# Performance work log

Hardware: AMD Instinct MI355X
Metric: run time of the kernel (lower is better)

## Reference

```python
import jax, jax.numpy as jnp
import numpy as np
from jax import lax

B, CIN, COUT, K = 4, 128, 128, 3
Z = X = Y = 32
EPS = 1e-8


def setup_inputs() -> dict:
    key = jax.random.key(0)
    k1, k2, k3 = jax.random.split(key, 3)
    x = jax.random.normal(k1, (B, CIN, Z, X, Y), dtype=jnp.float32)
    S = jax.random.normal(k2, (B, CIN), dtype=jnp.float32)
    weight = jax.random.normal(k3, (COUT, CIN, K, K, K), dtype=jnp.float32)
    return {"x": x, "S": S, "weight": weight}


def reference(x, S, weight):
    b, cin, z, xx, yy = x.shape
    cout = weight.shape[0]
    # Per-sample modulated weight: [B, cout, cin, k, k, k]
    W = weight[None] * (S[:, None, :, None, None, None] + 1.0)
    # Demodulation: L2-normalize each (b, cout) filter
    d = lax.rsqrt(jnp.sum(W * W, axis=(2, 3, 4, 5), keepdims=True) + EPS)
    W = W * d
    # Grouped conv3d with groups=B (stride=1, dilation=1 -> same padding = (k-1)//2)
    pad = (K - 1) // 2
    xr = x.reshape(1, b * cin, z, xx, yy)
    Wr = W.reshape(b * cout, cin, K, K, K)
    out = lax.conv_general_dilated(
        xr, Wr,
        window_strides=(1, 1, 1),
        padding=[(pad, pad)] * 3,
        feature_group_count=b,
        dimension_numbers=("NCDHW", "OIDHW", "NCDHW"),
    )
    return out.reshape(b, cout, z, xx, yy)
```

## Files before the change

### kernel.cpp

```cpp
#include <hip/hip_runtime.h>

#define B_    4
#define CIN_  128
#define COUT_ 128
#define EPSF  1e-8f

typedef short  short8  __attribute__((ext_vector_type(8)));
typedef unsigned short ushort8 __attribute__((ext_vector_type(8)));
typedef float  f32x16  __attribute__((ext_vector_type(16)));

__device__ __forceinline__ unsigned short f2bf(float f) {
    union { float f; unsigned int u; } v; v.f = f;
    unsigned int r = (v.u + 0x7fffu + ((v.u >> 16) & 1u)) >> 16;
    return (unsigned short)r;
}

__global__ __launch_bounds__(256) void prep_kernel(const float* __restrict__ x,
                                                   const float* __restrict__ S,
                                                   const float* __restrict__ w,
                                                   unsigned short* __restrict__ xT,
                                                   unsigned short* __restrict__ wtf,
                                                   float* __restrict__ dscale) {
    __shared__ float ls[128 * 33];
    const int bx  = blockIdx.x;
    const int tid = threadIdx.x;

    if (bx < 4096) {
        const int xx = bx & 31, z = (bx >> 5) & 31, b = bx >> 10;
        const size_t base = (size_t)b * 4194304 + (size_t)z * 1024 + xx * 32;
#pragma unroll
        for (int it = 0; it < 4; ++it) {
            int i = tid + it * 256;
            int ci = i >> 3, y4 = (i & 7) * 4;
            float4 v = *(const float4*)(x + base + (size_t)ci * 32768 + y4);
            float s = S[b * CIN_ + ci] + 1.0f;
            ls[ci * 33 + y4 + 0] = v.x * s;
            ls[ci * 33 + y4 + 1] = v.y * s;
            ls[ci * 33 + y4 + 2] = v.z * s;
            ls[ci * 33 + y4 + 3] = v.w * s;
        }
        __syncthreads();
        const size_t obase = (size_t)((b * 32 + z) * 32 + xx) * 4096;
#pragma unroll
        for (int it = 0; it < 2; ++it) {
            int i = tid + it * 256;
            int y = i >> 4, c = (i >> 1) & 7, h = i & 1;
            ushort8 v;
#pragma unroll
            for (int j = 0; j < 8; ++j) v[j] = f2bf(ls[(c * 16 + h * 8 + j) * 33 + y]);
            *(ushort8*)(xT + obase + c * 512 + y * 16 + h * 8) = v;
        }
    } else if (bx < 5824) {
        int idx = (bx - 4096) * 256 + tid;
        int e  = idx & 7;
        int l  = (idx >> 3) & 63;
        int c  = (idx >> 9) & 7;
        int ct = (idx >> 12) & 3;
        int ko = idx >> 14;
        int co = ct * 32 + (l & 31);
        int ci = c * 16 + (l >> 5) * 8 + e;
        wtf[idx] = f2bf(w[((size_t)co * CIN_ + ci) * 27 + ko]);
    } else {
        const int co = bx - 5824;
        const int ci = tid & 127;
        const float* wp = w + ((size_t)co * CIN_ + ci) * 27;
        float wsq = 0.f;
#pragma unroll
        for (int k = 0; k < 27; ++k) { float v = wp[k]; wsq += v * v; }
        for (int b = 0; b < B_; ++b) {
            float s = S[b * CIN_ + ci] + 1.0f;
            ls[ci] = s * s * wsq;
            __syncthreads();
            for (int off = 64; off > 0; off >>= 1) {
                if (tid < off) ls[tid] += ls[tid + off];
                __syncthreads();
            }
            if (tid == 0) dscale[b * COUT_ + co] = rsqrtf(ls[0] + EPSF);
            __syncthreads();
        }
    }
}

__global__ __launch_bounds__(256, 2) void conv_mfma(const unsigned short* __restrict__ xT,
                                                    const unsigned short* __restrict__ wtf,
                                                    const float* __restrict__ dscale,
                                                    float* __restrict__ out) {
    __shared__ char smem[2][26112];
    const int tid  = threadIdx.x;
    const int lane = tid & 63;
    const int wv   = tid >> 6;
    const int z0 = (blockIdx.x >> 4) * 4;
    const int x0 = (blockIdx.x & 15) * 2;
    const int b  = blockIdx.y;

    int goff[7];
    const int lbase = tid * 16;
#pragma unroll
    for (int s = 0; s < 7; ++s) {
        int g = tid + s * 256;
        goff[s] = -2;
        if (g < 1632) {
            int row = g / 68, rem = g - row * 68;
            int h = rem / 34, yi = rem - h * 34;
            int zg = z0 + (row >> 2) - 1;
            int xg = x0 + (row & 3) - 1;
            goff[s] = -1;
            if ((unsigned)zg < 32u && (unsigned)xg < 32u && yi >= 1 && yi <= 32)
                goff[s] = ((b * 32 + zg) * 32 + xg) * 8192 + (yi - 1) * 32 + h * 16;
        }
    }

    const char* xTb = (const char*)xT;
    const char* wtb = (const char*)wtf;
    const int bperlane = ((lane >> 5) * 34 + (lane & 31)) * 16;
    const int aperlane = lane * 16;

    f32x16 acc[4][2];
#pragma unroll
    for (int cz = 0; cz < 4; ++cz)
#pragma unroll
        for (int cx = 0; cx < 2; ++cx)
#pragma unroll
            for (int r = 0; r < 16; ++r) acc[cz][cx][r] = 0.f;

    ushort8 st[7];
#pragma unroll
    for (int s = 0; s < 7; ++s) {
        ushort8 v = {0, 0, 0, 0, 0, 0, 0, 0};
        if (goff[s] >= 0) v = *(const ushort8*)(xTb + goff[s]);
        st[s] = v;
    }
#pragma unroll
    for (int s = 0; s < 7; ++s)
        if (goff[s] != -2) *(ushort8*)(&smem[0][0] + lbase + s * 4096) = st[s];
    __syncthreads();

    for (int c = 0; c < 8; ++c) {
        if (c < 7) {
#pragma unroll
            for (int s = 0; s < 7; ++s) {
                ushort8 v = {0, 0, 0, 0, 0, 0, 0, 0};
                if (goff[s] >= 0) v = *(const ushort8*)(xTb + goff[s] + (c + 1) * 1024);
                st[s] = v;
            }
        }
        const char* buf   = smem[c & 1];
        const char* abase = wtb + c * 1024 + wv * 8192;
#pragma unroll
        for (int ky = 0; ky < 3; ++ky) {
            short8 a[9];
#pragma unroll
            for (int t = 0; t < 9; ++t)
                a[t] = *(const short8*)(abase + (t * 3 + ky) * 32768 + aperlane);
#pragma unroll
            for (int zr = 0; zr < 6; ++zr) {
                short8 bf[4];
#pragma unroll
                for (int xr = 0; xr < 4; ++xr)
                    bf[xr] = *(const short8*)(buf + ((zr * 4 + xr) * 68 + ky) * 16 + bperlane);
#pragma unroll
                for (int cz = 0; cz < 4; ++cz) {
                    const int kz = zr - cz;
                    if (kz >= 0 && kz <= 2) {
#pragma unroll
                        for (int cx = 0; cx < 2; ++cx)
#pragma unroll
                        for (int kx = 0; kx < 3; ++kx)
                            acc[cz][cx] = __builtin_amdgcn_mfma_f32_32x32x16_bf16(
                                a[kz * 3 + kx], bf[cx + kx], acc[cz][cx], 0, 0, 0);
                    }
                }
            }
        }
        if (c < 7) {
            char* nbuf = (char*)smem[(c + 1) & 1];
#pragma unroll
            for (int s = 0; s < 7; ++s)
                if (goff[s] != -2) *(ushort8*)(nbuf + lbase + s * 4096) = st[s];
        }
        __syncthreads();
    }

    float dd[16];
#pragma unroll
    for (int r = 0; r < 16; ++r)
        dd[r] = dscale[b * COUT_ + wv * 32 + (r & 3) + 8 * (r >> 2) + 4 * (lane >> 5)];
#pragma unroll
    for (int cz = 0; cz < 4; ++cz)
#pragma unroll
    for (int cx = 0; cx < 2; ++cx) {
        size_t ob = (((size_t)(b * COUT_ + wv * 32) * 32 + (z0 + cz)) * 32 + (x0 + cx)) * 32 + (lane & 31);
#pragma unroll
        for (int r = 0; r < 16; ++r) {
            int row = (r & 3) + 8 * (r >> 2) + 4 * (lane >> 5);
            out[ob + (size_t)row * 32768] = acc[cz][cx][r] * dd[r];
        }
    }
}

__global__ __launch_bounds__(256, 4) void conv_kernel(const float* __restrict__ x,
                                                      const float* __restrict__ S,
                                                      const float* __restrict__ w,
                                                      const float* __restrict__ dscale,
                                                      float* __restrict__ out) {
    __shared__ float xs[6][6][36];
    __shared__ float wsm[27][16];
    const int tid = threadIdx.x;
    const int zt  = blockIdx.x >> 3;
    const int xt  = blockIdx.x & 7;
    const int co0 = blockIdx.y * 16;
    const int b   = blockIdx.z;
    const int z0 = zt * 4, x0 = xt * 4;
    const int lane = tid & 63;
    const int cg = tid >> 6;
    const int zz = (lane >> 4) & 3;
    const int xx = (lane >> 2) & 3;
    const int y0 = (lane & 3) * 8;
    float acc[4][8];
#pragma unroll
    for (int c = 0; c < 4; ++c)
#pragma unroll
        for (int j = 0; j < 8; ++j) acc[c][j] = 0.f;
    for (int ci = 0; ci < CIN_; ++ci) {
        __syncthreads();
        const float* xb = x + (size_t)(b * CIN_ + ci) * 32768;
        const float smod = S[b * CIN_ + ci] + 1.0f;
#pragma unroll
        for (int t = 0; t < 5; ++t) {
            int i = tid + t * 256;
            if (i < 6 * 6 * 34) {
                int zi = i / 204, r = i - zi * 204, xi = r / 34, yi = r - xi * 34;
                int z = z0 + zi - 1, xc = x0 + xi - 1, y = yi - 1;
                float v = 0.f;
                if ((unsigned)z < 32u && (unsigned)xc < 32u && (unsigned)y < 32u)
                    v = xb[z * 1024 + xc * 32 + y] * smod;
                xs[zi][xi][yi] = v;
            }
        }
#pragma unroll
        for (int t = 0; t < 2; ++t) {
            int i = tid + t * 256;
            if (i < 16 * 27) {
                int cog2 = i / 27, k = i - cog2 * 27;
                wsm[k][cog2] = w[((size_t)(co0 + cog2) * CIN_ + ci) * 27 + k];
            }
        }
        __syncthreads();
#pragma unroll
        for (int kz = 0; kz < 3; ++kz)
#pragma unroll
        for (int kx = 0; kx < 3; ++kx) {
            const float* xrow = &xs[zz + kz][xx + kx][y0];
            float xw[10];
#pragma unroll
            for (int q = 0; q < 10; ++q) xw[q] = xrow[q];
            const int kb = (kz * 3 + kx) * 3;
#pragma unroll
            for (int ky = 0; ky < 3; ++ky) {
                float4 wvv = *(const float4*)&wsm[kb + ky][cg * 4];
#pragma unroll
                for (int j = 0; j < 8; ++j) {
                    acc[0][j] = fmaf(xw[ky + j], wvv.x, acc[0][j]);
                    acc[1][j] = fmaf(xw[ky + j], wvv.y, acc[1][j]);
                    acc[2][j] = fmaf(xw[ky + j], wvv.z, acc[2][j]);
                    acc[3][j] = fmaf(xw[ky + j], wvv.w, acc[3][j]);
                }
            }
        }
    }
#pragma unroll
    for (int c = 0; c < 4; ++c) {
        const int co = co0 + cg * 4 + c;
        const float dd = dscale[b * COUT_ + co];
        float* ob = out + (((size_t)(b * COUT_ + co) * 32 + (z0 + zz)) * 32 + (x0 + xx)) * 32 + y0;
#pragma unroll
        for (int j = 0; j < 8; ++j) ob[j] = acc[c][j] * dd;
    }
}

__global__ __launch_bounds__(128) void scale_only_kernel(const float* __restrict__ S,
                                                         const float* __restrict__ w,
                                                         float* __restrict__ d) {
    const int co = blockIdx.x;
    const int ci = threadIdx.x;
    const float* wp = w + ((size_t)co * CIN_ + ci) * 27;
    float wsq = 0.f;
#pragma unroll
    for (int k = 0; k < 27; ++k) { float v = wp[k]; wsq += v * v; }
    __shared__ float red[128];
    for (int b = 0; b < B_; ++b) {
        float s = S[b * CIN_ + ci] + 1.0f;
        red[ci] = s * s * wsq;
        __syncthreads();
        for (int off = 64; off > 0; off >>= 1) {
            if (ci < off) red[ci] += red[ci + off];
            __syncthreads();
        }
        if (ci == 0) d[b * COUT_ + co] = rsqrtf(red[0] + EPSF);
        __syncthreads();
    }
}

extern "C" void kernel_launch(void* const* d_in, const int* in_sizes, int n_in,
                              void* d_out, int out_size, void* d_ws, size_t ws_size,
                              hipStream_t stream) {
    const float* x = (const float*)d_in[0];
    const float* S = (const float*)d_in[1];
    const float* w = (const float*)d_in[2];
    float* out = (float*)d_out;

    const size_t NEED = 1048576 + 33554432;
    if (ws_size >= NEED) {
        float* dscale = (float*)d_ws;
        unsigned short* wtf = (unsigned short*)((char*)d_ws + 4096);
        unsigned short* xT  = (unsigned short*)((char*)d_ws + 1048576);
        prep_kernel<<<dim3(5952), dim3(256), 0, stream>>>(x, S, w, xT, wtf, dscale);
        conv_mfma<<<dim3(128, 4), dim3(256), 0, stream>>>(xT, wtf, dscale, out);
    } else {
        float* dscale = (float*)d_ws;
        scale_only_kernel<<<dim3(COUT_), dim3(128), 0, stream>>>(S, w, dscale);
        conv_kernel<<<dim3(64, 8, 4), dim3(256), 0, stream>>>(x, S, w, dscale, out);
    }
}
```

Before: 111.3 us.

## Stage input tiles with direct global-to-LDS loads and halve z tile

```diff
diff --git a/kernel.cpp b/kernel.cpp
--- a/kernel.cpp
+++ b/kernel.cpp
@@ -8,6 +8,10 @@
 typedef short  short8  __attribute__((ext_vector_type(8)));
 typedef unsigned short ushort8 __attribute__((ext_vector_type(8)));
 typedef float  f32x16  __attribute__((ext_vector_type(16)));
+
+#define GLOAD_LDS16(g, l) __builtin_amdgcn_global_load_lds( \
+    (const __attribute__((address_space(1))) unsigned int*)(g), \
+    (__attribute__((address_space(3))) unsigned int*)(l), 16, 0, 0)
 
 __device__ __forceinline__ unsigned short f2bf(float f) {
     union { float f; unsigned int u; } v; v.f = f;
@@ -81,115 +85,110 @@
     }
 }
 
-__global__ __launch_bounds__(256, 2) void conv_mfma(const unsigned short* __restrict__ xT,
-                                                    const unsigned short* __restrict__ wtf,
-                                                    const float* __restrict__ dscale,
-                                                    float* __restrict__ out) {
-    __shared__ char smem[2][26112];
+__global__ __launch_bounds__(256, 4) void conv_mfma4(const unsigned short* __restrict__ xT,
+                                                     const unsigned short* __restrict__ wtf,
+                                                     const float* __restrict__ dscale,
+                                                     float* __restrict__ out) {
+    __shared__ char smem[2][17408];
     const int tid  = threadIdx.x;
     const int lane = tid & 63;
-    const int wv   = tid >> 6;
-    const int z0 = (blockIdx.x >> 4) * 4;
+    const int cog  = tid >> 6;
+    const int z0 = (blockIdx.x >> 4) * 2;
     const int x0 = (blockIdx.x & 15) * 2;
     const int b  = blockIdx.y;
 
-    int goff[7];
-    const int lbase = tid * 16;
-#pragma unroll
-    for (int s = 0; s < 7; ++s) {
-        int g = tid + s * 256;
-        goff[s] = -2;
-        if (g < 1632) {
-            int row = g / 68, rem = g - row * 68;
-            int h = rem / 34, yi = rem - h * 34;
-            int zg = z0 + (row >> 2) - 1;
-            int xg = x0 + (row & 3) - 1;
-            goff[s] = -1;
-            if ((unsigned)zg < 32u && (unsigned)xg < 32u && yi >= 1 && yi <= 32)
-                goff[s] = ((b * 32 + zg) * 32 + xg) * 8192 + (yi - 1) * 32 + h * 16;
-        }
-    }
-
-    const char* xTb = (const char*)xT;
+    const char* xbase = (const char*)xT - 8192;
+
+    unsigned int off[5];
+#pragma unroll
+    for (int s = 0; s < 5; ++s) {
+        int g = (s < 4) ? (tid + s * 256) : (1024 + tid);
+        int row = g / 68, rem = g - row * 68;
+        int h = rem / 34, yi = rem - h * 34;
+        int zg = z0 + (row >> 2) - 1;
+        int xg = x0 + (row & 3) - 1;
+        bool ok = (g < 1088) && ((unsigned)zg < 32u) && ((unsigned)xg < 32u) &&
+                  (yi >= 1) && (yi <= 32);
+        off[s] = ok ? (unsigned)(8192 + ((b * 32 + zg) * 32 + xg) * 8192 +
+                                 (yi - 1) * 32 + h * 16)
+                    : 0u;
+    }
+
     const char* wtb = (const char*)wtf;
     const int bperlane = ((lane >> 5) * 34 + (lane & 31)) * 16;
     const int aperlane = lane * 16;
 
-    f32x16 acc[4][2];
-#pragma unroll
-    for (int cz = 0; cz < 4; ++cz)
+    f32x16 acc[2][2];
+#pragma unroll
+    for (int cz = 0; cz < 2; ++cz)
 #pragma unroll
         for (int cx = 0; cx < 2; ++cx)
 #pragma unroll
             for (int r = 0; r < 16; ++r) acc[cz][cx][r] = 0.f;
 
-    ushort8 st[7];
-#pragma unroll
-    for (int s = 0; s < 7; ++s) {
-        ushort8 v = {0, 0, 0, 0, 0, 0, 0, 0};
-        if (goff[s] >= 0) v = *(const ushort8*)(xTb + goff[s]);
-        st[s] = v;
-    }
-#pragma unroll
-    for (int s = 0; s < 7; ++s)
-        if (goff[s] != -2) *(ushort8*)(&smem[0][0] + lbase + s * 4096) = st[s];
+#define STAGE_CHUNK(NB, COFF)                                                   \
+    {                                                                           \
+        _Pragma("unroll")                                                       \
+        for (int s = 0; s < 4; ++s)                                             \
+            GLOAD_LDS16(xbase + off[s] + (COFF), &smem[NB][tid * 16 + s * 4096]); \
+        if (tid < 64)                                                           \
+            GLOAD_LDS16(xbase + off[4] + (COFF), &smem[NB][16384 + tid * 16]);  \
+    }
+
+    STAGE_CHUNK(0, 0)
     __syncthreads();
 
     for (int c = 0; c < 8; ++c) {
-        if (c < 7) {
-#pragma unroll
-            for (int s = 0; s < 7; ++s) {
-                ushort8 v = {0, 0, 0, 0, 0, 0, 0, 0};
-                if (goff[s] >= 0) v = *(const ushort8*)(xTb + goff[s] + (c + 1) * 1024);
-                st[s] = v;
-            }
-        }
+        if (c < 7) STAGE_CHUNK((c + 1) & 1, (c + 1) * 1024)
         const char* buf   = smem[c & 1];
-        const char* abase = wtb + c * 1024 + wv * 8192;
-#pragma unroll
-        for (int ky = 0; ky < 3; ++ky) {
-            short8 a[9];
-#pragma unroll
-            for (int t = 0; t < 9; ++t)
-                a[t] = *(const short8*)(abase + (t * 3 + ky) * 32768 + aperlane);
-#pragma unroll
-            for (int zr = 0; zr < 6; ++zr) {
+        const char* abase = wtb + c * 1024 + cog * 8192;
+
+        short8 ap[2][3];
+#pragma unroll
+        for (int kx = 0; kx < 3; ++kx)
+            ap[0][kx] = *(const short8*)(abase + (kx * 3 + 0) * 32768 + aperlane);
+
+#pragma unroll
+        for (int p = 0; p < 9; ++p) {
+            const int ky = p / 3, kz = p % 3;
+            const int cur = p & 1, nxt = cur ^ 1;
+            if (p < 8) {
+                const int ky2 = (p + 1) / 3, kz2 = (p + 1) % 3;
+#pragma unroll
+                for (int kx = 0; kx < 3; ++kx)
+                    ap[nxt][kx] = *(const short8*)(abase +
+                        ((kz2 * 3 + kx) * 3 + ky2) * 32768 + aperlane);
+            }
+#pragma unroll
+            for (int cz = 0; cz < 2; ++cz) {
+                const int zr = kz + cz;
                 short8 bf[4];
 #pragma unroll
                 for (int xr = 0; xr < 4; ++xr)
                     bf[xr] = *(const short8*)(buf + ((zr * 4 + xr) * 68 + ky) * 16 + bperlane);
-#pragma unroll
-                for (int cz = 0; cz < 4; ++cz) {
-                    const int kz = zr - cz;
-                    if (kz >= 0 && kz <= 2) {
-#pragma unroll
-                        for (int cx = 0; cx < 2; ++cx)
-#pragma unroll
-                        for (int kx = 0; kx < 3; ++kx)
-                            acc[cz][cx] = __builtin_amdgcn_mfma_f32_32x32x16_bf16(
-                                a[kz * 3 + kx], bf[cx + kx], acc[cz][cx], 0, 0, 0);
-                    }
-                }
-            }
-        }
-        if (c < 7) {
-            char* nbuf = (char*)smem[(c + 1) & 1];
-#pragma unroll
-            for (int s = 0; s < 7; ++s)
-                if (goff[s] != -2) *(ushort8*)(nbuf + lbase + s * 4096) = st[s];
-        }
-        __syncthreads();
-    }
+                __builtin_amdgcn_s_setprio(1);
+                acc[cz][0] = __builtin_amdgcn_mfma_f32_32x32x16_bf16(ap[cur][0], bf[0], acc[cz][0], 0, 0, 0);
+                acc[cz][1] = __builtin_amdgcn_mfma_f32_32x32x16_bf16(ap[cur][0], bf[1], acc[cz][1], 0, 0, 0);
+                acc[cz][0] = __builtin_amdgcn_mfma_f32_32x32x16_bf16(ap[cur][1], bf[1], acc[cz][0], 0, 0, 0);
+                acc[cz][1] = __builtin_amdgcn_mfma_f32_32x32x16_bf16(ap[cur][1], bf[2], acc[cz][1], 0, 0, 0);
+                acc[cz][0] = __builtin_amdgcn_mfma_f32_32x32x16_bf16(ap[cur][2], bf[2], acc[cz][0], 0, 0, 0);
+                acc[cz][1] = __builtin_amdgcn_mfma_f32_32x32x16_bf16(ap[cur][2], bf[3], acc[cz][1], 0, 0, 0);
+                __builtin_amdgcn_s_setprio(0);
+            }
+        }
+        __syncthreads();
+    }
+#undef STAGE_CHUNK
 
     float dd[16];
 #pragma unroll
     for (int r = 0; r < 16; ++r)
-        dd[r] = dscale[b * COUT_ + wv * 32 + (r & 3) + 8 * (r >> 2) + 4 * (lane >> 5)];
-#pragma unroll
-    for (int cz = 0; cz < 4; ++cz)
+        dd[r] = dscale[b * COUT_ + cog * 32 + (r & 3) + 8 * (r >> 2) + 4 * (lane >> 5)];
+#pragma unroll
+    for (int cz = 0; cz < 2; ++cz)
 #pragma unroll
     for (int cx = 0; cx < 2; ++cx) {
-        size_t ob = (((size_t)(b * COUT_ + wv * 32) * 32 + (z0 + cz)) * 32 + (x0 + cx)) * 32 + (lane & 31);
+        size_t ob = (((size_t)(b * COUT_ + cog * 32) * 32 + (z0 + cz)) * 32 + (x0 + cx)) * 32 + (lane & 31);
 #pragma unroll
         for (int r = 0; r < 16; ++r) {
             int row = (r & 3) + 8 * (r >> 2) + 4 * (lane >> 5);
@@ -313,9 +312,11 @@
     if (ws_size >= NEED) {
         float* dscale = (float*)d_ws;
         unsigned short* wtf = (unsigned short*)((char*)d_ws + 4096);
+        char*  zpage  = (char*)d_ws + 1048576 - 8192;
         unsigned short* xT  = (unsigned short*)((char*)d_ws + 1048576);
+        hipMemsetAsync(zpage, 0, 8192, stream);
         prep_kernel<<<dim3(5952), dim3(256), 0, stream>>>(x, S, w, xT, wtf, dscale);
-        conv_mfma<<<dim3(128, 4), dim3(256), 0, stream>>>(xT, wtf, dscale, out);
+        conv_mfma4<<<dim3(256, 4), dim3(256), 0, stream>>>(xT, wtf, dscale, out);
     } else {
         float* dscale = (float*)d_ws;
         scale_only_kernel<<<dim3(COUT_), dim3(128), 0, stream>>>(S, w, dscale);
```

After: 125.3 us. 1.13x slower.

## Pre-pad input in workspace and stream conv operands directly from global memory

Applied to the files above, without the earlier changes.

```diff
diff --git a/kernel.cpp b/kernel.cpp
--- a/kernel.cpp
+++ b/kernel.cpp
@@ -13,6 +13,182 @@
     union { float f; unsigned int u; } v; v.f = f;
     unsigned int r = (v.u + 0x7fffu + ((v.u >> 16) & 1u)) >> 16;
     return (unsigned short)r;
+}
+
+__global__ __launch_bounds__(256) void prep2_kernel(const float* __restrict__ x,
+                                                    const float* __restrict__ S,
+                                                    const float* __restrict__ w,
+                                                    unsigned short* __restrict__ xT2,
+                                                    unsigned short* __restrict__ wtf,
+                                                    float* __restrict__ dscale) {
+    __shared__ float ls[128 * 33];
+    const int bx  = blockIdx.x;
+    const int tid = threadIdx.x;
+    const ushort8 z8 = {0, 0, 0, 0, 0, 0, 0, 0};
+
+    if (bx < 4624) {
+        const int b  = bx / 1156;
+        const int r  = bx - b * 1156;
+        const int zp = r / 34, xp = r - zp * 34;
+        unsigned short* row = xT2 + (size_t)bx * 4352;
+        if (zp == 0 || zp == 33 || xp == 0 || xp == 33) {
+#pragma unroll
+            for (int it = 0; it < 2; ++it) {
+                int i = tid + it * 256;
+                *(ushort8*)(row + i * 8) = z8;
+            }
+            if (tid < 32) *(ushort8*)(row + (512 + tid) * 8) = z8;
+            return;
+        }
+        const int z = zp - 1, xx = xp - 1;
+        const size_t base = (size_t)b * 4194304 + (size_t)z * 1024 + xx * 32;
+#pragma unroll
+        for (int it = 0; it < 4; ++it) {
+            int i = tid + it * 256;
+            int ci = i >> 3, y4 = (i & 7) * 4;
+            float4 v = *(const float4*)(x + base + (size_t)ci * 32768 + y4);
+            float s = S[b * CIN_ + ci] + 1.0f;
+            ls[ci * 33 + y4 + 0] = v.x * s;
+            ls[ci * 33 + y4 + 1] = v.y * s;
+            ls[ci * 33 + y4 + 2] = v.z * s;
+            ls[ci * 33 + y4 + 3] = v.w * s;
+        }
+        __syncthreads();
+#pragma unroll
+        for (int it = 0; it < 2; ++it) {
+            int i = tid + it * 256;
+            int y = i >> 4, c = (i >> 1) & 7, h = i & 1;
+            ushort8 v;
+#pragma unroll
+            for (int j = 0; j < 8; ++j) v[j] = f2bf(ls[(c * 16 + h * 8 + j) * 33 + y]);
+            *(ushort8*)(row + c * 544 + (y + 1) * 16 + h * 8) = v;
+        }
+        if (tid < 32) {
+            int c = tid >> 2, h = (tid >> 1) & 1, yp = (tid & 1) * 33;
+            *(ushort8*)(row + c * 544 + yp * 16 + h * 8) = z8;
+        }
+    } else if (bx < 6352) {
+        int idx = (bx - 4624) * 256 + tid;
+        int e  = idx & 7;
+        int l  = (idx >> 3) & 63;
+        int c  = (idx >> 9) & 7;
+        int ct = (idx >> 12) & 3;
+        int ko = idx >> 14;
+        int co = ct * 32 + (l & 31);
+        int ci = c * 16 + (l >> 5) * 8 + e;
+        wtf[idx] = f2bf(w[((size_t)co * CIN_ + ci) * 27 + ko]);
+    } else {
+        const int co = bx - 6352;
+        const int ci = tid & 127;
+        const float* wp = w + ((size_t)co * CIN_ + ci) * 27;
+        float wsq = 0.f;
+#pragma unroll
+        for (int k = 0; k < 27; ++k) { float v = wp[k]; wsq += v * v; }
+        for (int b = 0; b < B_; ++b) {
+            float s = S[b * CIN_ + ci] + 1.0f;
+            ls[ci] = s * s * wsq;
+            __syncthreads();
+            for (int off = 64; off > 0; off >>= 1) {
+                if (tid < off) ls[tid] += ls[tid + off];
+                __syncthreads();
+            }
+            if (tid == 0) dscale[b * COUT_ + co] = rsqrtf(ls[0] + EPSF);
+            __syncthreads();
+        }
+    }
+}
+
+__global__ __launch_bounds__(256, 2) void conv_stream(const unsigned short* __restrict__ xT2,
+                                                      const unsigned short* __restrict__ wtf,
+                                                      const float* __restrict__ dscale,
+                                                      float* __restrict__ out) {
+    const int tid  = threadIdx.x;
+    const int lane = tid & 63;
+    const int wv   = tid >> 6;
+    const int z0 = (blockIdx.x >> 4) * 4;
+    const int x0 = (blockIdx.x & 15) * 2;
+    const int b  = blockIdx.y;
+
+    const char* bsp = (const char*)xT2 + ((size_t)b * 1156 + (size_t)z0 * 34 + x0) * 8704;
+    const char* wtb = (const char*)wtf;
+    const int bper = (lane & 31) * 32 + (lane >> 5) * 16;
+    const int aper = lane * 16;
+
+    f32x16 acc[4][2];
+#pragma unroll
+    for (int cz = 0; cz < 4; ++cz)
+#pragma unroll
+        for (int cx = 0; cx < 2; ++cx)
+#pragma unroll
+            for (int r = 0; r < 16; ++r) acc[cz][cx][r] = 0.f;
+
+    for (int c = 0; c < 8; ++c) {
+        const char* abase = wtb + c * 1024 + wv * 8192;
+        const char* xb    = bsp + c * 1088;
+
+        short8 bf[3][4];
+#pragma unroll
+        for (int xr = 0; xr < 4; ++xr)
+            bf[0][xr] = *(const short8*)(xb + (0 * 34 + xr) * 8704 + 0 * 32 + bper);
+#pragma unroll
+        for (int xr = 0; xr < 4; ++xr)
+            bf[1][xr] = *(const short8*)(xb + (1 * 34 + xr) * 8704 + 0 * 32 + bper);
+
+#pragma unroll
+        for (int ky = 0; ky < 3; ++ky) {
+            short8 a[9];
+#pragma unroll
+            for (int t = 0; t < 9; ++t)
+                a[t] = *(const short8*)(abase + (t * 3 + ky) * 32768 + aper);
+#pragma unroll
+            for (int zr = 0; zr < 6; ++zr) {
+                if (zr < 4) {
+#pragma unroll
+                    for (int xr = 0; xr < 4; ++xr)
+                        bf[(zr + 2) % 3][xr] = *(const short8*)(xb +
+                            ((zr + 2) * 34 + xr) * 8704 + ky * 32 + bper);
+                } else if (ky < 2) {
+#pragma unroll
+                    for (int xr = 0; xr < 4; ++xr)
+                        bf[(zr + 2) % 3][xr] = *(const short8*)(xb +
+                            ((zr - 4) * 34 + xr) * 8704 + (ky + 1) * 32 + bper);
+                }
+                __builtin_amdgcn_s_setprio(1);
+                {
+                    const short8* bb = bf[zr % 3];
+#pragma unroll
+                    for (int cz = 0; cz < 4; ++cz) {
+                        const int kz = zr - cz;
+                        if (kz >= 0 && kz <= 2) {
+                            acc[cz][0] = __builtin_amdgcn_mfma_f32_32x32x16_bf16(a[kz*3+0], bb[0], acc[cz][0], 0,0,0);
+                            acc[cz][1] = __builtin_amdgcn_mfma_f32_32x32x16_bf16(a[kz*3+0], bb[1], acc[cz][1], 0,0,0);
+                            acc[cz][0] = __builtin_amdgcn_mfma_f32_32x32x16_bf16(a[kz*3+1], bb[1], acc[cz][0], 0,0,0);
+                            acc[cz][1] = __builtin_amdgcn_mfma_f32_32x32x16_bf16(a[kz*3+1], bb[2], acc[cz][1], 0,0,0);
+                            acc[cz][0] = __builtin_amdgcn_mfma_f32_32x32x16_bf16(a[kz*3+2], bb[2], acc[cz][0], 0,0,0);
+                            acc[cz][1] = __builtin_amdgcn_mfma_f32_32x32x16_bf16(a[kz*3+2], bb[3], acc[cz][1], 0,0,0);
+                        }
+                    }
+                }
+                __builtin_amdgcn_s_setprio(0);
+            }
+        }
+    }
+
+    float dd[16];
+#pragma unroll
+    for (int r = 0; r < 16; ++r)
+        dd[r] = dscale[b * COUT_ + wv * 32 + (r & 3) + 8 * (r >> 2) + 4 * (lane >> 5)];
+#pragma unroll
+    for (int cz = 0; cz < 4; ++cz)
+#pragma unroll
+    for (int cx = 0; cx < 2; ++cx) {
+        size_t ob = (((size_t)(b * COUT_ + wv * 32) * 32 + (z0 + cz)) * 32 + (x0 + cx)) * 32 + (lane & 31);
+#pragma unroll
+        for (int r = 0; r < 16; ++r) {
+            int row = (r & 3) + 8 * (r >> 2) + 4 * (lane >> 5);
+            out[ob + (size_t)row * 32768] = acc[cz][cx][r] * dd[r];
+        }
+    }
 }
 
 __global__ __launch_bounds__(256) void prep_kernel(const float* __restrict__ x,
@@ -24,7 +200,6 @@
     __shared__ float ls[128 * 33];
     const int bx  = blockIdx.x;
     const int tid = threadIdx.x;
-
     if (bx < 4096) {
         const int xx = bx & 31, z = (bx >> 5) & 31, b = bx >> 10;
         const size_t base = (size_t)b * 4194304 + (size_t)z * 1024 + xx * 32;
@@ -52,11 +227,8 @@
         }
     } else if (bx < 5824) {
         int idx = (bx - 4096) * 256 + tid;
-        int e  = idx & 7;
-        int l  = (idx >> 3) & 63;
-        int c  = (idx >> 9) & 7;
-        int ct = (idx >> 12) & 3;
-        int ko = idx >> 14;
+        int e = idx & 7, l = (idx >> 3) & 63, c = (idx >> 9) & 7;
+        int ct = (idx >> 12) & 3, ko = idx >> 14;
         int co = ct * 32 + (l & 31);
         int ci = c * 16 + (l >> 5) * 8 + e;
         wtf[idx] = f2bf(w[((size_t)co * CIN_ + ci) * 27 + ko]);
@@ -109,7 +281,6 @@
                 goff[s] = ((b * 32 + zg) * 32 + xg) * 8192 + (yi - 1) * 32 + h * 16;
         }
     }
-
     const char* xTb = (const char*)xT;
     const char* wtb = (const char*)wtf;
     const int bperlane = ((lane >> 5) * 34 + (lane & 31)) * 16;
@@ -154,10 +325,10 @@
                 a[t] = *(const short8*)(abase + (t * 3 + ky) * 32768 + aperlane);
 #pragma unroll
             for (int zr = 0; zr < 6; ++zr) {
-                short8 bf[4];
+                short8 bfv[4];
 #pragma unroll
                 for (int xr = 0; xr < 4; ++xr)
-                    bf[xr] = *(const short8*)(buf + ((zr * 4 + xr) * 68 + ky) * 16 + bperlane);
+                    bfv[xr] = *(const short8*)(buf + ((zr * 4 + xr) * 68 + ky) * 16 + bperlane);
 #pragma unroll
                 for (int cz = 0; cz < 4; ++cz) {
                     const int kz = zr - cz;
@@ -167,7 +338,7 @@
 #pragma unroll
                         for (int kx = 0; kx < 3; ++kx)
                             acc[cz][cx] = __builtin_amdgcn_mfma_f32_32x32x16_bf16(
-                                a[kz * 3 + kx], bf[cx + kx], acc[cz][cx], 0, 0, 0);
+                                a[kz * 3 + kx], bfv[cx + kx], acc[cz][cx], 0, 0, 0);
                     }
                 }
             }
@@ -309,8 +480,15 @@
     const float* w = (const float*)d_in[2];
     float* out = (float*)d_out;
 
-    const size_t NEED = 1048576 + 33554432;
-    if (ws_size >= NEED) {
+    const size_t NEED_PAD = 1048576 + 40247296;
+    const size_t NEED_STD = 1048576 + 33554432;
+    if (ws_size >= NEED_PAD) {
+        float* dscale = (float*)d_ws;
+        unsigned short* wtf = (unsigned short*)((char*)d_ws + 4096);
+        unsigned short* xT2 = (unsigned short*)((char*)d_ws + 1048576);
+        prep2_kernel<<<dim3(6480), dim3(256), 0, stream>>>(x, S, w, xT2, wtf, dscale);
+        conv_stream<<<dim3(128, 4), dim3(256), 0, stream>>>(xT2, wtf, dscale, out);
+    } else if (ws_size >= NEED_STD) {
         float* dscale = (float*)d_ws;
         unsigned short* wtf = (unsigned short*)((char*)d_ws + 4096);
         unsigned short* xT  = (unsigned short*)((char*)d_ws + 1048576);
```

Result: slower. 148.5 us (+33.4%).
